# Optimization experiments

Hardware: AMD Instinct MI355X
Metric: run time of the kernel (lower is better)

Reference implementation:

```python
import jax, jax.numpy as jnp
import numpy as np

B, L, D, E, K, P = 1024, 320, 128, 8, 2, 96
NOISE_EPS = 0.01
LOSS_COEF = 0.01


def setup_inputs() -> dict:
    key = jax.random.key(0)
    ks = jax.random.split(key, 8)
    return {
        "x": jax.random.normal(ks[0], (B, L, D), jnp.float32),
        "x_mark_enc": jax.random.normal(ks[1], (B, L, 4), jnp.float32),
        "noise": jax.random.normal(ks[2], (B, E), jnp.float32),  # randn_like in torch
        "start_w": jax.random.normal(ks[3], (D, 1), jnp.float32) * 0.05,
        "start_b": jnp.zeros((1,), jnp.float32),
        "w_gate": jax.random.normal(ks[4], (L, E), jnp.float32) * 0.02,
        "w_noise": jax.random.normal(ks[5], (L, E), jnp.float32) * 0.02,
        "expert_w": jax.random.normal(ks[6], (E, L, P), jnp.float32) * (1.0 / np.sqrt(L)),
        "expert_b": jnp.zeros((E, P, D), jnp.float32),
    }


def _norm_cdf(v):
    return 0.5 * (1.0 + jax.lax.erf(v * (1.0 / np.sqrt(2.0)).astype(v.dtype) if hasattr((1.0 / np.sqrt(2.0)), 'astype') else v / jnp.sqrt(jnp.asarray(2.0, v.dtype))))


def _cdf(v):
    # standard normal CDF, Normal(0,1).cdf
    return 0.5 * (1.0 + jax.lax.erf(v / jnp.sqrt(jnp.asarray(2.0, v.dtype))))


def _cv_squared(v):
    eps = 1e-10
    return jnp.var(v, ddof=1) / (jnp.mean(v) ** 2 + eps)


def reference(x, x_mark_enc, noise, start_w, start_b, w_gate, w_noise, expert_b, expert_w):
    # --- noisy top-k gating (train mode) ---
    g = jnp.squeeze(x @ start_w, -1) + start_b  # [B, L]
    clean_logits = g @ w_gate                    # [B, E]
    noise_std = jax.nn.softplus(g @ w_noise) + NOISE_EPS
    noisy_logits = clean_logits + noise * noise_std

    top_logits, top_idx = jax.lax.top_k(noisy_logits, K + 1)  # [B, K+1]
    top_k_gates = jax.nn.softmax(top_logits[:, :K], axis=1)
    gates = jnp.zeros_like(noisy_logits).at[
        jnp.arange(noisy_logits.shape[0])[:, None], top_idx[:, :K]
    ].set(top_k_gates)  # [B, E] sparse gates (zeros elsewhere)

    # --- differentiable load via prob-in-top-k ---
    thr_in = top_logits[:, K:K + 1]       # (k+1)-th noisy value
    thr_out = top_logits[:, K - 1:K]      # k-th noisy value
    clean_c = jnp.where(jnp.isnan(clean_logits), 0.0, clean_logits)
    prob = jnp.where(
        noisy_logits > thr_in,
        _cdf((clean_c - thr_in) / noise_std),
        _cdf((clean_c - thr_out) / noise_std),
    )
    load = prob.sum(0)          # [E]
    importance = gates.sum(0)   # [E]
    balance_loss = LOSS_COEF * (_cv_squared(importance) + _cv_squared(load))

    # --- dispatch/combine: dense-equivalent of SparseDispatcher ---
    # expert e: out_e = einsum('bld,lp->bpd', x, W_e); combine weights = gates
    per_expert = jnp.einsum('bld,elp->ebpd', x, expert_w)          # [E, B, P, D]
    out = jnp.einsum('be,ebpd->bpd', gates, per_expert)
    out = out + jnp.einsum('be,epd->bpd', gates, expert_b)
    regu_sum = jnp.asarray(0.0, jnp.float32)
    return out, balance_loss, regu_sum
```

## Files before the change

### kernel.cpp

```cpp
#include <hip/hip_runtime.h>
#include <hip/hip_bf16.h>

#define Bn 1024
#define Lr 320
#define Dd 128
#define Ee 8
#define Pp 96

typedef short bf16x8 __attribute__((ext_vector_type(8)));
typedef float f32x4 __attribute__((ext_vector_type(4)));
typedef unsigned u32x4 __attribute__((ext_vector_type(4)));
typedef unsigned short u16;

__device__ __forceinline__ float cdf_f(float v) {
    return 0.5f * (1.0f + erff(v * 0.70710678118654752f));
}
__device__ __forceinline__ float softplus_f(float x) {
    return fmaxf(x, 0.0f) + log1pf(expf(-fabsf(x)));
}
__device__ __forceinline__ u16 f2bf(float f) {
    unsigned int u = __float_as_uint(f);
    return (u16)((u + 0x7fffu + ((u >> 16) & 1u)) >> 16);
}
__device__ __forceinline__ float bf2f(u16 u) {
    return __uint_as_float(((unsigned int)u) << 16);
}

__device__ __forceinline__ void gload16(const void* g, void* l) {
    __builtin_amdgcn_global_load_lds(
        (const __attribute__((address_space(1))) void*)g,
        (__attribute__((address_space(3))) void*)l, 16, 0, 0);
}

__global__ __launch_bounds__(256) void transpose_w(
    const float* __restrict__ ew, u16* __restrict__ wt,
    float* __restrict__ accum)
{
    __shared__ float tile[Pp * 33];
    const int e  = blockIdx.x;
    const int l0 = blockIdx.y * 32;
    const int t  = threadIdx.x;
    if (e == 0 && blockIdx.y == 0 && t < 16) accum[t] = 0.f;
    #pragma unroll
    for (int i = 0; i < 12; ++i) {
        const int idx = t + 256 * i;
        const int lp = idx / 96, p = idx - 96 * lp;
        tile[p * 33 + lp] = ew[((size_t)e * Lr + l0 + lp) * Pp + p];
    }
    __syncthreads();
    #pragma unroll
    for (int i = 0; i < 6; ++i) {
        const int g = t + 256 * i;
        const int p = g >> 4, l2 = (g & 15) * 2;
        const unsigned pk = (unsigned)f2bf(tile[p * 33 + l2]) |
                            ((unsigned)f2bf(tile[p * 33 + l2 + 1]) << 16);
        *(unsigned*)&wt[((size_t)(e * Pp + p)) * Lr + l0 + l2] = pk;
    }
}

__global__ __launch_bounds__(256, 8) void g_kernel(
    const float* __restrict__ x, const float* __restrict__ start_w,
    const float* __restrict__ start_b, float* __restrict__ g_out)
{
    const int t  = threadIdx.x;
    const int lc = blockIdx.x;
    const int b  = blockIdx.y;
    const float sb = start_b[0];

    float4 sw[4];
    #pragma unroll
    for (int j = 0; j < 4; ++j) sw[j] = ((const float4*)start_w)[(t & 7) + 8 * j];

    const float* xb = x + ((size_t)b * Lr + lc * 64) * Dd;
    #pragma unroll
    for (int p2 = 0; p2 < 2; ++p2) {
        const int r = p2 * 32 + (t >> 3);
        float acc = 0.f;
        #pragma unroll
        for (int j = 0; j < 4; ++j) {
            const float4 v = ((const float4*)(xb + (size_t)r * Dd))[(t & 7) + 8 * j];
            acc += v.x * sw[j].x + v.y * sw[j].y + v.z * sw[j].z + v.w * sw[j].w;
        }
        #pragma unroll
        for (int off = 1; off <= 4; off <<= 1) acc += __shfl_xor(acc, off);
        if ((t & 7) == 0) g_out[(size_t)b * Lr + lc * 64 + r] = acc + sb;
    }
}

__global__ __launch_bounds__(256) void gate_kernel(
    const float* __restrict__ g, const float* __restrict__ noise,
    const float* __restrict__ w_gate, const float* __restrict__ w_noise,
    float* __restrict__ accum, float* __restrict__ gates_out)
{
    __shared__ float sred[16];
    const int t    = threadIdx.x;
    const int lane = t & 63;
    const int wv   = t >> 6;
    const int b    = blockIdx.x * 4 + wv;

    if (t < 16) sred[t] = 0.f;
    __syncthreads();

    const int e = lane & 7, seg = lane >> 3;
    const float* gb = g + (size_t)b * Lr;
    float pc = 0.f, pn = 0.f;
    #pragma unroll 8
    for (int i = 0; i < 40; ++i) {
        const int l = seg * 40 + i;
        const float gv = gb[l];
        pc += gv * w_gate[l * Ee + e];
        pn += gv * w_noise[l * Ee + e];
    }
    #pragma unroll
    for (int off = 8; off <= 32; off <<= 1) {
        pc += __shfl_xor(pc, off);
        pn += __shfl_xor(pn, off);
    }
    const float sdv   = softplus_f(pn) + 0.01f;
    float       c     = pc;
    const float nz    = noise[b * Ee + e];
    const float noisy = c + nz * sdv;

    float nv[8];
    #pragma unroll
    for (int j = 0; j < 8; ++j) nv[j] = __shfl(noisy, j);

    int i0 = -1, i1 = -1;
    float v0 = -INFINITY, v1 = -INFINITY, v2 = -INFINITY;
    #pragma unroll
    for (int i = 0; i < 8; ++i) if (nv[i] > v0) { v0 = nv[i]; i0 = i; }
    #pragma unroll
    for (int i = 0; i < 8; ++i) if (i != i0 && nv[i] > v1) { v1 = nv[i]; i1 = i; }
    #pragma unroll
    for (int i = 0; i < 8; ++i) if (i != i0 && i != i1 && nv[i] > v2) { v2 = nv[i]; }

    const float ex1 = expf(v1 - v0);
    const float den = 1.f + ex1;
    const float gate_e = (e == i0) ? (1.f / den) : ((e == i1) ? (ex1 / den) : 0.f);

    if (isnan(c)) c = 0.f;
    const float pr = (noisy > v2) ? cdf_f((c - v2) / sdv) : cdf_f((c - v1) / sdv);

    if (lane < 8) {
        gates_out[b * Ee + e] = gate_e;
        atomicAdd(&sred[8 + e], gate_e);
        atomicAdd(&sred[e], pr);
    }
    __syncthreads();
    if (t < 16) atomicAdd(&accum[t], sred[t]);
}

__global__ __launch_bounds__(256, 4) void mm_kernel(
    const float* __restrict__ x, const u16* __restrict__ wt,
    const float* __restrict__ expert_b, const float* __restrict__ gates,
    const float* __restrict__ accum, float* __restrict__ out)
{
    __shared__ __align__(16) unsigned Ws[2][192 * 16];

    const int tid  = threadIdx.x;

    if (blockIdx.x == 0 && tid == 0) {
        float lo[8], im[8];
        #pragma unroll
        for (int i = 0; i < 8; ++i) { lo[i] = accum[i]; im[i] = accum[8 + i]; }
        float ml = 0.f, mi = 0.f;
        #pragma unroll
        for (int i = 0; i < 8; ++i) { ml += lo[i]; mi += im[i]; }
        ml *= 0.125f; mi *= 0.125f;
        float sl = 0.f, si = 0.f;
        #pragma unroll
        for (int i = 0; i < 8; ++i) {
            const float dl = lo[i] - ml, di = im[i] - mi;
            sl += dl * dl; si += di * di;
        }
        const float cvl = (sl / 7.f) / (ml * ml + 1e-10f);
        const float cvi = (si / 7.f) / (mi * mi + 1e-10f);
        float* os = out + (size_t)Bn * Pp * Dd;
        os[0] = 0.01f * (cvi + cvl);
        os[1] = 0.0f;
    }

    const int b    = blockIdx.x >> 1;
    const int h    = blockIdx.x & 1;
    const int lane = tid & 63;
    const int wv   = tid >> 6;
    const int quad = lane >> 4;
    const int r16  = lane & 15;

    int e0 = 0, e1 = 0; float g0 = 0.f, g1 = 0.f; int cnt = 0;
    #pragma unroll
    for (int e = 0; e < Ee; ++e) {
        const float gv = gates[b * Ee + e];
        if (gv != 0.f) {
            if (cnt == 0) { e0 = e; g0 = gv; }
            else if (cnt == 1) { e1 = e; g1 = gv; }
            ++cnt;
        }
    }

    const u16* w0r = wt + (size_t)e0 * Pp * Lr;
    const u16* w1r = wt + (size_t)e1 * Pp * Lr;

    const int d = h * 64 + 16 * wv + r16;
    const float* xg = x + ((size_t)b * Lr + 8 * quad) * Dd + d;

    const int wrow = lane >> 2;
    const int wq   = lane & 3;

    auto STAGE_W = [&](int buf, int l0) {
        #pragma unroll
        for (int i = 0; i < 3; ++i) {
            const int c  = 3 * wv + i;
            const int r  = 16 * c + wrow;
            const int dw = (4 * wq) ^ ((r & 3) << 2);
            const u16* src = (c < 6) ? (w0r + (size_t)r * Lr)
                                     : (w1r + (size_t)(r - 96) * Lr);
            gload16(src + l0 + 2 * dw, (void*)&Ws[buf][c * 256]);
        }
    };

    float xa[8], xb8[8];
    auto LOADX = [&](float* dst, int l0) {
        #pragma unroll
        for (int k = 0; k < 8; ++k)
            dst[k] = xg[(size_t)(l0 + k) * Dd];
    };

    f32x4 a0[6], a1[6];
    #pragma unroll
    for (int m = 0; m < 6; ++m) {
        a0[m] = (f32x4){0.f, 0.f, 0.f, 0.f};
        a1[m] = (f32x4){0.f, 0.f, 0.f, 0.f};
    }

    const int wdw = (4 * quad) ^ ((r16 & 3) << 2);

    union UF { u32x4 q; bf16x8 v; unsigned u[4]; };

    auto COMPUTE = [&](int buf, const float* xv) {
        UF xf;
        #pragma unroll
        for (int k2 = 0; k2 < 4; ++k2)
            xf.u[k2] = (unsigned)f2bf(xv[2 * k2]) |
                       ((unsigned)f2bf(xv[2 * k2 + 1]) << 16);
        #pragma unroll
        for (int m = 0; m < 6; ++m) {
            UF f0, f1;
            f0.q = *(const u32x4*)&Ws[buf][(16 * m + r16) * 16 + wdw];
            f1.q = *(const u32x4*)&Ws[buf][(96 + 16 * m + r16) * 16 + wdw];
            a0[m] = __builtin_amdgcn_mfma_f32_16x16x32_bf16(f0.v, xf.v, a0[m], 0, 0, 0);
            a1[m] = __builtin_amdgcn_mfma_f32_16x16x32_bf16(f1.v, xf.v, a1[m], 0, 0, 0);
        }
    };

    STAGE_W(0, 0);
    LOADX(xa, 0);
    __syncthreads();

    #pragma unroll
    for (int t = 0; t < 10; t += 2) {
        STAGE_W(1, 32 * (t + 1));
        LOADX(xb8, 32 * (t + 1));
        COMPUTE(0, xa);
        __syncthreads();
        if (t + 2 < 10) {
            STAGE_W(0, 32 * (t + 2));
            LOADX(xa, 32 * (t + 2));
        }
        COMPUTE(1, xb8);
        __syncthreads();
    }

    const float* eb0 = expert_b + (size_t)e0 * Pp * Dd;
    const float* eb1 = expert_b + (size_t)e1 * Pp * Dd;
    #pragma unroll
    for (int m = 0; m < 6; ++m) {
        #pragma unroll
        for (int r = 0; r < 4; ++r) {
            const int p = 16 * m + 4 * quad + r;
            out[((size_t)b * Pp + p) * Dd + d] =
                g0 * (a0[m][r] + eb0[p * Dd + d]) +
                g1 * (a1[m][r] + eb1[p * Dd + d]);
        }
    }
}

extern "C" void kernel_launch(void* const* d_in, const int* in_sizes, int n_in,
                              void* d_out, int out_size, void* d_ws, size_t ws_size,
                              hipStream_t stream)
{
    const float* x        = (const float*)d_in[0];
    const float* noise    = (const float*)d_in[2];
    const float* start_w  = (const float*)d_in[3];
    const float* start_b  = (const float*)d_in[4];
    const float* w_gate   = (const float*)d_in[5];
    const float* w_noise  = (const float*)d_in[6];
    const float* expert_w = (const float*)d_in[7];
    const float* expert_b = (const float*)d_in[8];
    float* out            = (float*)d_out;

    float* accum = (float*)d_ws;
    float* gates = accum + 16;
    float* gbuf  = gates + Bn * Ee;
    u16*   wt    = (u16*)(gbuf + Bn * Lr);

    hipLaunchKernelGGL(transpose_w, dim3(Ee, Lr / 32), dim3(256), 0, stream,
                       expert_w, wt, accum);
    hipLaunchKernelGGL(g_kernel, dim3(5, Bn), dim3(256), 0, stream,
                       x, start_w, start_b, gbuf);
    hipLaunchKernelGGL(gate_kernel, dim3(Bn / 4), dim3(256), 0, stream,
                       gbuf, noise, w_gate, w_noise, accum, gates);
    hipLaunchKernelGGL(mm_kernel, dim3(Bn * 2), dim3(256), 0, stream,
                       x, wt, expert_b, gates, accum, out);
}
```

Measured before the change: 304.8 us.

## Fuse gate projection into g kernel and make top-k one thread per row

```diff
diff --git a/kernel.cpp b/kernel.cpp
--- a/kernel.cpp
+++ b/kernel.cpp
@@ -34,13 +34,17 @@
 
 __global__ __launch_bounds__(256) void transpose_w(
     const float* __restrict__ ew, u16* __restrict__ wt,
-    float* __restrict__ accum)
+    float* __restrict__ accum, float* __restrict__ zbuf)
 {
     __shared__ float tile[Pp * 33];
     const int e  = blockIdx.x;
     const int l0 = blockIdx.y * 32;
     const int t  = threadIdx.x;
     if (e == 0 && blockIdx.y == 0 && t < 16) accum[t] = 0.f;
+    {
+        const int idx = (blockIdx.x * 10 + blockIdx.y) * 256 + t;
+        if (idx < Bn * 16) zbuf[idx] = 0.f;
+    }
     #pragma unroll
     for (int i = 0; i < 12; ++i) {
         const int idx = t + 256 * i;
@@ -58,93 +62,117 @@
     }
 }
 
-__global__ __launch_bounds__(256, 8) void g_kernel(
+__global__ __launch_bounds__(256, 8) void g2_kernel(
     const float* __restrict__ x, const float* __restrict__ start_w,
-    const float* __restrict__ start_b, float* __restrict__ g_out)
-{
+    const float* __restrict__ start_b, const float* __restrict__ w_gate,
+    const float* __restrict__ w_noise, float* __restrict__ zbuf)
+{
+    __shared__ float sred[16];
     const int t  = threadIdx.x;
     const int lc = blockIdx.x;
     const int b  = blockIdx.y;
     const float sb = start_b[0];
+    const int f8 = t & 7;
+
+    if (t < 16) sred[t] = 0.f;
+    __syncthreads();
 
     float4 sw[4];
     #pragma unroll
-    for (int j = 0; j < 4; ++j) sw[j] = ((const float4*)start_w)[(t & 7) + 8 * j];
+    for (int j = 0; j < 4; ++j) sw[j] = ((const float4*)start_w)[f8 + 8 * j];
 
     const float* xb = x + ((size_t)b * Lr + lc * 64) * Dd;
+    float zc = 0.f, zn = 0.f;
     #pragma unroll
     for (int p2 = 0; p2 < 2; ++p2) {
         const int r = p2 * 32 + (t >> 3);
         float acc = 0.f;
         #pragma unroll
         for (int j = 0; j < 4; ++j) {
-            const float4 v = ((const float4*)(xb + (size_t)r * Dd))[(t & 7) + 8 * j];
+            const float4 v = ((const float4*)(xb + (size_t)r * Dd))[f8 + 8 * j];
             acc += v.x * sw[j].x + v.y * sw[j].y + v.z * sw[j].z + v.w * sw[j].w;
         }
         #pragma unroll
         for (int off = 1; off <= 4; off <<= 1) acc += __shfl_xor(acc, off);
-        if ((t & 7) == 0) g_out[(size_t)b * Lr + lc * 64 + r] = acc + sb;
-    }
-}
-
-__global__ __launch_bounds__(256) void gate_kernel(
-    const float* __restrict__ g, const float* __restrict__ noise,
-    const float* __restrict__ w_gate, const float* __restrict__ w_noise,
+        const float gv = acc + sb;
+        const int l = lc * 64 + r;
+        zc += gv * w_gate[l * Ee + f8];
+        zn += gv * w_noise[l * Ee + f8];
+    }
+    #pragma unroll
+    for (int off = 8; off <= 32; off <<= 1) {
+        zc += __shfl_xor(zc, off);
+        zn += __shfl_xor(zn, off);
+    }
+    if ((t & 63) < 8) {
+        atomicAdd(&sred[f8], zc);
+        atomicAdd(&sred[8 + f8], zn);
+    }
+    __syncthreads();
+    if (t < 16) atomicAdd(&zbuf[b * 16 + t], sred[t]);
+}
+
+__global__ __launch_bounds__(256) void topk_kernel(
+    const float* __restrict__ zbuf, const float* __restrict__ noise,
     float* __restrict__ accum, float* __restrict__ gates_out)
 {
     __shared__ float sred[16];
-    const int t    = threadIdx.x;
-    const int lane = t & 63;
-    const int wv   = t >> 6;
-    const int b    = blockIdx.x * 4 + wv;
+    const int t = threadIdx.x;
+    const int b = blockIdx.x * 256 + t;
 
     if (t < 16) sred[t] = 0.f;
     __syncthreads();
 
-    const int e = lane & 7, seg = lane >> 3;
-    const float* gb = g + (size_t)b * Lr;
-    float pc = 0.f, pn = 0.f;
-    #pragma unroll 8
-    for (int i = 0; i < 40; ++i) {
-        const int l = seg * 40 + i;
-        const float gv = gb[l];
-        pc += gv * w_gate[l * Ee + e];
-        pn += gv * w_noise[l * Ee + e];
-    }
-    #pragma unroll
-    for (int off = 8; off <= 32; off <<= 1) {
-        pc += __shfl_xor(pc, off);
-        pn += __shfl_xor(pn, off);
-    }
-    const float sdv   = softplus_f(pn) + 0.01f;
-    float       c     = pc;
-    const float nz    = noise[b * Ee + e];
-    const float noisy = c + nz * sdv;
-
-    float nv[8];
-    #pragma unroll
-    for (int j = 0; j < 8; ++j) nv[j] = __shfl(noisy, j);
+    float zc[8], zn[8], nsy[8], sdv[8];
+    #pragma unroll
+    for (int e = 0; e < 8; ++e) {
+        zc[e] = zbuf[b * 16 + e];
+        zn[e] = zbuf[b * 16 + 8 + e];
+    }
+    #pragma unroll
+    for (int e = 0; e < 8; ++e) {
+        sdv[e] = softplus_f(zn[e]) + 0.01f;
+        nsy[e] = zc[e] + noise[b * Ee + e] * sdv[e];
+    }
 
     int i0 = -1, i1 = -1;
     float v0 = -INFINITY, v1 = -INFINITY, v2 = -INFINITY;
     #pragma unroll
-    for (int i = 0; i < 8; ++i) if (nv[i] > v0) { v0 = nv[i]; i0 = i; }
-    #pragma unroll
-    for (int i = 0; i < 8; ++i) if (i != i0 && nv[i] > v1) { v1 = nv[i]; i1 = i; }
-    #pragma unroll
-    for (int i = 0; i < 8; ++i) if (i != i0 && i != i1 && nv[i] > v2) { v2 = nv[i]; }
+    for (int i = 0; i < 8; ++i) if (nsy[i] > v0) { v0 = nsy[i]; i0 = i; }
+    #pragma unroll
+    for (int i = 0; i < 8; ++i) if (i != i0 && nsy[i] > v1) { v1 = nsy[i]; i1 = i; }
+    #pragma unroll
+    for (int i = 0; i < 8; ++i) if (i != i0 && i != i1 && nsy[i] > v2) { v2 = nsy[i]; }
 
     const float ex1 = expf(v1 - v0);
     const float den = 1.f + ex1;
-    const float gate_e = (e == i0) ? (1.f / den) : ((e == i1) ? (ex1 / den) : 0.f);
-
-    if (isnan(c)) c = 0.f;
-    const float pr = (noisy > v2) ? cdf_f((c - v2) / sdv) : cdf_f((c - v1) / sdv);
-
-    if (lane < 8) {
-        gates_out[b * Ee + e] = gate_e;
-        atomicAdd(&sred[8 + e], gate_e);
-        atomicAdd(&sred[e], pr);
+    const float g0 = 1.f / den, g1 = ex1 / den;
+
+    float im[8], pr[8];
+    #pragma unroll
+    for (int e = 0; e < 8; ++e) {
+        im[e] = (e == i0) ? g0 : ((e == i1) ? g1 : 0.f);
+        float c = zc[e];
+        if (isnan(c)) c = 0.f;
+        pr[e] = (nsy[e] > v2) ? cdf_f((c - v2) / sdv[e])
+                              : cdf_f((c - v1) / sdv[e]);
+        gates_out[b * Ee + e] = im[e];
+    }
+
+    #pragma unroll
+    for (int off = 1; off <= 32; off <<= 1) {
+        #pragma unroll
+        for (int e = 0; e < 8; ++e) {
+            pr[e] += __shfl_xor(pr[e], off);
+            im[e] += __shfl_xor(im[e], off);
+        }
+    }
+    if ((t & 63) == 0) {
+        #pragma unroll
+        for (int e = 0; e < 8; ++e) {
+            atomicAdd(&sred[e], pr[e]);
+            atomicAdd(&sred[8 + e], im[e]);
+        }
     }
     __syncthreads();
     if (t < 16) atomicAdd(&accum[t], sred[t]);
@@ -301,15 +329,15 @@
 
     float* accum = (float*)d_ws;
     float* gates = accum + 16;
-    float* gbuf  = gates + Bn * Ee;
-    u16*   wt    = (u16*)(gbuf + Bn * Lr);
+    float* zbuf  = gates + Bn * Ee;
+    u16*   wt    = (u16*)(zbuf + Bn * 16);
 
     hipLaunchKernelGGL(transpose_w, dim3(Ee, Lr / 32), dim3(256), 0, stream,
-                       expert_w, wt, accum);
-    hipLaunchKernelGGL(g_kernel, dim3(5, Bn), dim3(256), 0, stream,
-                       x, start_w, start_b, gbuf);
-    hipLaunchKernelGGL(gate_kernel, dim3(Bn / 4), dim3(256), 0, stream,
-                       gbuf, noise, w_gate, w_noise, accum, gates);
+                       expert_w, wt, accum, zbuf);
+    hipLaunchKernelGGL(g2_kernel, dim3(5, Bn), dim3(256), 0, stream,
+                       x, start_w, start_b, w_gate, w_noise, zbuf);
+    hipLaunchKernelGGL(topk_kernel, dim3(Bn / 256), dim3(256), 0, stream,
+                       zbuf, noise, accum, gates);
     hipLaunchKernelGGL(mm_kernel, dim3(Bn * 2), dim3(256), 0, stream,
                        x, wt, expert_b, gates, accum, out);
 }
```

After: 306.2 us. About the same (+0.5%).
